# Performance work log

Measured on AMD Instinct MI355X. Metric: run time of the kernel, lower is better.

Reference implementation:

```python
import jax, jax.numpy as jnp
import numpy as np

NUM_HEADS = 12


def _rel_pos_table(q_size, k_size, rel_pos):
    # rel_pos: (2*q_size-1, head_dim); q_size == k_size here so no interpolation.
    q_coords = jnp.arange(q_size)[:, None] * max(k_size / q_size, 1.0)
    k_coords = jnp.arange(k_size)[None, :] * max(q_size / k_size, 1.0)
    rel = (q_coords - k_coords + (k_size - 1) * max(q_size / k_size, 1.0)).astype(jnp.int32)
    return rel_pos[rel]  # (q_size, k_size, head_dim)


def setup_inputs() -> dict:
    key = jax.random.key(0)
    ks = jax.random.split(key, 7)
    B, H, W, D = 1, 64, 64, 768
    hd = D // NUM_HEADS
    x = jax.random.normal(ks[0], (B, H, W, D), dtype=jnp.float32)
    w_qkv = jax.random.normal(ks[1], (3 * D, D), dtype=jnp.float32) * (1.0 / np.sqrt(D))
    b_qkv = jnp.zeros((3 * D,), dtype=jnp.float32)
    w_proj = jax.random.normal(ks[2], (D, D), dtype=jnp.float32) * (1.0 / np.sqrt(D))
    b_proj = jnp.zeros((D,), dtype=jnp.float32)
    rel_pos_h = jax.random.normal(ks[3], (2 * H - 1, hd), dtype=jnp.float32) * 0.02
    rel_pos_w = jax.random.normal(ks[4], (2 * W - 1, hd), dtype=jnp.float32) * 0.02
    return {"x": x, "w_qkv": w_qkv, "b_qkv": b_qkv, "w_proj": w_proj,
            "b_proj": b_proj, "rel_pos_h": rel_pos_h, "rel_pos_w": rel_pos_w}


def reference(x, w_qkv, b_qkv, w_proj, b_proj, rel_pos_h, rel_pos_w):
    b, h, w, d = x.shape
    nh = NUM_HEADS
    hd = d // nh
    scale = hd ** -0.5
    # combined qkv projection: (b,h,w,3d) -> (3, b*nh, h*w, hd)
    qkv = x @ w_qkv.T + b_qkv
    qkv = qkv.reshape(b, h * w, 3, nh, hd).transpose(2, 0, 3, 1, 4)
    qkv = qkv.reshape(3, b * nh, h * w, hd)
    q, k, v = qkv[0], qkv[1], qkv[2]
    attn = (q * scale) @ k.swapaxes(-2, -1)  # (b*nh, hw, hw)
    # decomposed 2D relative position bias
    rh = _rel_pos_table(h, h, rel_pos_h)  # (h, h, hd)
    rw = _rel_pos_table(w, w, rel_pos_w)  # (w, w, hd)
    r_q = q.reshape(b * nh, h, w, hd)
    rel_h = jnp.einsum('bhwc,hkc->bhwk', r_q, rh)
    rel_w = jnp.einsum('bhwc,wkc->bhwk', r_q, rw)
    attn = (attn.reshape(b * nh, h, w, h, w)
            + rel_h[:, :, :, :, None]
            + rel_w[:, :, :, None, :]).reshape(b * nh, h * w, h * w)
    attn = jax.nn.softmax(attn, axis=-1)
    out = attn @ v  # (b*nh, hw, hd)
    out = out.reshape(b, nh, h, w, hd).transpose(0, 2, 3, 1, 4).reshape(b, h, w, d)
    return out @ w_proj.T + b_proj
```

## Files before the change

### kernel.cpp

```cpp
#include <hip/hip_runtime.h>
#include <hip/hip_bf16.h>
#include <stdint.h>


typedef unsigned short u16;
typedef unsigned int   u32;
typedef __attribute__((ext_vector_type(8))) short s8v;
typedef __attribute__((ext_vector_type(4))) float f4v;
typedef __attribute__((ext_vector_type(4))) unsigned short us4;
typedef __attribute__((ext_vector_type(8))) unsigned short us8;
typedef __attribute__((ext_vector_type(2))) unsigned int u32x2;

#define DEVI static __device__ __forceinline__

constexpr int   NTOK   = 4096;
constexpr int   DM     = 768;
constexpr float LOG2E_F = 1.4426950408889634f;
constexpr float KSCALE  = 0.18033688011112042f;

#if __has_builtin(__builtin_amdgcn_exp2f)
#define EXP2(x) __builtin_amdgcn_exp2f(x)
#else
#define EXP2(x) exp2f(x)
#endif

DEVI u16 f2bf(float x){
  u32 u = __builtin_bit_cast(u32, x);
  u32 r = (u + 0x7FFFu + ((u >> 16) & 1u)) >> 16;
  return (u16)r;
}
DEVI float bf2f(u16 h){
  u32 u = ((u32)h) << 16;
  return __builtin_bit_cast(float, u);
}
DEVI u32 cvtpk(float lo, float hi){
  u32 r;
  asm("v_cvt_pk_bf16_f32 %0, %1, %2" : "=v"(r) : "v"(lo), "v"(hi));
  return r;
}

typedef const __attribute__((address_space(1))) u32* gp1;
typedef __attribute__((address_space(3))) u32* lp3;
DEVI void gload_lds16(const void* g, void* l){
  __builtin_amdgcn_global_load_lds((gp1)g, (lp3)l, 16, 0, 0);
}

DEVI f4v MFMA16(s8v a, s8v b, f4v c){
  return __builtin_amdgcn_mfma_f32_16x16x32_bf16(a, b, c, 0, 0, 0);
}

DEVI void hard_barrier(){
  __builtin_amdgcn_sched_barrier(0);
  asm volatile("" ::: "memory");
  __builtin_amdgcn_s_barrier();
  asm volatile("" ::: "memory");
  __builtin_amdgcn_sched_barrier(0);
}

__global__ void k_split(const float* __restrict__ in, u16* __restrict__ hi,
                        u16* __restrict__ lo, int n4){
  int i = blockIdx.x * blockDim.x + threadIdx.x;
  int stride = gridDim.x * blockDim.x;
  for (; i < n4; i += stride){
    f4v v = ((const f4v*)in)[i];
    us4 h, l;
#pragma unroll
    for (int j = 0; j < 4; ++j){
      u16 hb = f2bf(v[j]);
      h[j] = hb;
      l[j] = f2bf(v[j] - bf2f(hb));
    }
    ((us4*)hi)[i] = h;
    ((us4*)lo)[i] = l;
  }
}

template<int EPI>
__global__ __launch_bounds__(256)
void k_gemm(const u16* __restrict__ Ah, const u16* __restrict__ Al,
            const u16* __restrict__ Bh, const u16* __restrict__ Bl,
            const float* __restrict__ bias, int K,
            u16* __restrict__ Qh, u16* __restrict__ Ql,
            u16* __restrict__ Kh, u16* __restrict__ Kl,
            float* __restrict__ Vf, float* __restrict__ Cout)
{
  __shared__ __align__(16) unsigned char sm[65536];
  const int t = threadIdx.x;
  const int lane = t & 63, wid = t >> 6;
  const int l15 = lane & 15, g = lane >> 4;
  const int wr = wid >> 1, wc = wid & 1;
  const int m0 = blockIdx.y * 128, n0 = blockIdx.x * 128;

  const char* aGh[2]; const char* aGl[2]; const char* bGh[2]; const char* bGl[2];
#pragma unroll
  for (int ch = 0; ch < 2; ++ch){
    int p = ch * 4096 + t * 16;
    int pair = p >> 7, w = p & 127;
    int u = w ^ ((pair & 7) << 4);
    int row = 2 * pair + (u >> 6);
    int cb  = u & 63;
    aGh[ch] = (const char*)Ah + (size_t)(m0 + row) * K * 2 + cb;
    aGl[ch] = (const char*)Al + (size_t)(m0 + row) * K * 2 + cb;
    bGh[ch] = (const char*)Bh + (size_t)(n0 + row) * K * 2 + cb;
    bGl[ch] = (const char*)Bl + (size_t)(n0 + row) * K * 2 + cb;
  }
  const int axor = ((l15 & 1) * 64 + g * 16) ^ (((l15 >> 1) & 7) << 4);
  const int abase = (wr * 32 + (l15 >> 1)) * 128 + axor;
  const int bbase = 16384 + (wc * 32 + (l15 >> 1)) * 128 + axor;

#pragma unroll
  for (int ch = 0; ch < 2; ++ch){
    gload_lds16(aGh[ch], sm + 0     + ch*4096 + wid*1024);
    gload_lds16(aGl[ch], sm + 8192  + ch*4096 + wid*1024);
    gload_lds16(bGh[ch], sm + 16384 + ch*4096 + wid*1024);
    gload_lds16(bGl[ch], sm + 24576 + ch*4096 + wid*1024);
    aGh[ch] += 64; aGl[ch] += 64; bGh[ch] += 64; bGl[ch] += 64;
  }

  f4v acc[4][4] = {};
  const int KSTEPS = K >> 5;
  for (int kt = 0; kt < KSTEPS; ++kt){
    const int bb = (kt & 1) * 32768;
    if (kt + 1 < KSTEPS){
      const int nb = ((kt + 1) & 1) * 32768;
#pragma unroll
      for (int ch = 0; ch < 2; ++ch){
        gload_lds16(aGh[ch], sm + nb + 0     + ch*4096 + wid*1024);
        gload_lds16(aGl[ch], sm + nb + 8192  + ch*4096 + wid*1024);
        gload_lds16(bGh[ch], sm + nb + 16384 + ch*4096 + wid*1024);
        gload_lds16(bGl[ch], sm + nb + 24576 + ch*4096 + wid*1024);
        aGh[ch] += 64; aGl[ch] += 64; bGh[ch] += 64; bGl[ch] += 64;
      }
      asm volatile("s_waitcnt vmcnt(8)" ::: "memory");
    } else {
      asm volatile("s_waitcnt vmcnt(0)" ::: "memory");
    }
    hard_barrier();

    s8v af[4][2];
#pragma unroll
    for (int mi = 0; mi < 4; ++mi){
      af[mi][0] = *(const s8v*)(sm + bb + abase + mi*1024);
      af[mi][1] = *(const s8v*)(sm + bb + abase + mi*1024 + 8192);
    }
    __builtin_amdgcn_s_setprio(1);
#pragma unroll
    for (int ni = 0; ni < 4; ++ni){
      s8v bh = *(const s8v*)(sm + bb + bbase + ni*1024);
      s8v bl = *(const s8v*)(sm + bb + bbase + ni*1024 + 8192);
#pragma unroll
      for (int mi = 0; mi < 4; ++mi){
        acc[mi][ni] = MFMA16(af[mi][0], bh, acc[mi][ni]);
        acc[mi][ni] = MFMA16(af[mi][0], bl, acc[mi][ni]);
        acc[mi][ni] = MFMA16(af[mi][1], bh, acc[mi][ni]);
      }
    }
    __builtin_amdgcn_s_setprio(0);
    hard_barrier();
  }

  if (EPI == 2){
#pragma unroll
    for (int ni = 0; ni < 4; ++ni){
      int col = n0 + wc*64 + ni*16 + l15;
      float bq = bias[col];
#pragma unroll
      for (int mi = 0; mi < 4; ++mi){
        int rw0 = m0 + wr*64 + mi*16 + g*4;
#pragma unroll
        for (int r = 0; r < 4; ++r)
          Cout[(size_t)(rw0 + r) * DM + col] = acc[mi][ni][r] + bq;
      }
    }
  } else {
#pragma unroll
    for (int ni = 0; ni < 4; ++ni){
      int colb = n0 + wc*64 + ni*16;
      float bq = bias[colb + l15];
      int which = colb / DM;
      int rem   = colb % DM;
      int head  = rem >> 6;
      int c     = (rem & 63) + l15;
#pragma unroll
      for (int mi = 0; mi < 4; ++mi){
        int n = m0 + wr*64 + mi*16 + g*4;
#pragma unroll
        for (int r = 0; r < 4; ++r){
          float v = acc[mi][ni][r] + bq;
          size_t idx = ((size_t)head * NTOK + (n + r)) * 64 + c;
          if (which == 0){
            u16 hb = f2bf(v);
            Qh[idx] = hb; Ql[idx] = f2bf(v - bf2f(hb));
          } else if (which == 1){
            float v2 = v * KSCALE;
            u16 hb = f2bf(v2);
            Kh[idx] = hb; Kl[idx] = f2bf(v2 - bf2f(hb));
          } else {
            Vf[idx] = v;
          }
        }
      }
    }
  }
}

__global__ void k_vtrans(const float* __restrict__ Vf, u16* __restrict__ Vth){
  __shared__ float tile[64][65];
  int h = blockIdx.y, nt = blockIdx.x;
  int t = threadIdx.x;
  {
    int r = t >> 2, c0 = (t & 3) * 16;
    const float* src = Vf + ((size_t)h * NTOK + nt*64 + r) * 64 + c0;
#pragma unroll
    for (int j = 0; j < 4; ++j){
      f4v v = *(const f4v*)(src + j*4);
      tile[r][c0+j*4+0] = v[0]; tile[r][c0+j*4+1] = v[1];
      tile[r][c0+j*4+2] = v[2]; tile[r][c0+j*4+3] = v[3];
    }
  }
  __syncthreads();
  {
    int c = t >> 2, b = (t & 3) * 16;
    us8 o0, o1;
#pragma unroll
    for (int i = 0; i < 16; ++i){
      u16 bv = f2bf(tile[b + i][c]);
      if (i < 8) o0[i] = bv; else o1[i-8] = bv;
    }
    u16* dst = Vth + ((size_t)h * 64 + c) * NTOK + nt*64 + b;
    *(us8*)(dst)     = o0;
    *(us8*)(dst + 8) = o1;
  }
}

__global__ void k_relh(const u16* __restrict__ Qh, const u16* __restrict__ Ql,
                       const float* __restrict__ rp, float* __restrict__ R){
  __shared__ float qs[64][68];
  __shared__ float rs[64][68];
  int h = blockIdx.y, qh = blockIdx.x;
  int t = threadIdx.x;
  {
    int r = t >> 2, c0 = (t & 3) * 16;
    size_t qb = ((size_t)h * NTOK + qh*64 + r) * 64 + c0;
#pragma unroll
    for (int j = 0; j < 2; ++j){
      us8 vh = *(const us8*)(Qh + qb + j*8);
      us8 vl = *(const us8*)(Ql + qb + j*8);
#pragma unroll
      for (int e = 0; e < 8; ++e)
        qs[r][c0 + j*8 + e] = bf2f(vh[e]) + bf2f(vl[e]);
    }
    const float* pr = rp + (size_t)(qh - r + 63) * 64 + c0;
#pragma unroll
    for (int j = 0; j < 4; ++j){
      f4v v = *(const f4v*)(pr + j*4);
      rs[r][c0+j*4+0]=v[0]; rs[r][c0+j*4+1]=v[1];
      rs[r][c0+j*4+2]=v[2]; rs[r][c0+j*4+3]=v[3];
    }
  }
  __syncthreads();
  int qw = t >> 2, k0 = t & 3;
  float acc[16] = {};
  for (int c = 0; c < 64; c += 4){
    f4v qv = *(const f4v*)(&qs[qw][c]);
#pragma unroll
    for (int i = 0; i < 16; ++i){
      f4v rv = *(const f4v*)(&rs[k0 + 4*i][c]);
      acc[i] += qv[0]*rv[0] + qv[1]*rv[1] + qv[2]*rv[2] + qv[3]*rv[3];
    }
  }
  float* o = R + ((size_t)h * NTOK + qh*64 + qw) * 64;
#pragma unroll
  for (int i = 0; i < 16; ++i) o[k0 + 4*i] = acc[i] * LOG2E_F;
}

__global__ void k_relw(const u16* __restrict__ Qh, const u16* __restrict__ Ql,
                       const float* __restrict__ rp, float* __restrict__ R){
  __shared__ float qs[64][68];
  __shared__ float rs[64][68];
  int h = blockIdx.y, qw = blockIdx.x;
  int t = threadIdx.x;
  {
    int r = t >> 2, c0 = (t & 3) * 16;
    size_t qb = ((size_t)h * NTOK + r*64 + qw) * 64 + c0;
#pragma unroll
    for (int j = 0; j < 2; ++j){
      us8 vh = *(const us8*)(Qh + qb + j*8);
      us8 vl = *(const us8*)(Ql + qb + j*8);
#pragma unroll
      for (int e = 0; e < 8; ++e)
        qs[r][c0 + j*8 + e] = bf2f(vh[e]) + bf2f(vl[e]);
    }
    const float* pr = rp + (size_t)(qw - r + 63) * 64 + c0;
#pragma unroll
    for (int j = 0; j < 4; ++j){
      f4v v = *(const f4v*)(pr + j*4);
      rs[r][c0+j*4+0]=v[0]; rs[r][c0+j*4+1]=v[1];
      rs[r][c0+j*4+2]=v[2]; rs[r][c0+j*4+3]=v[3];
    }
  }
  __syncthreads();
  int qh = t >> 2, k0 = t & 3;
  float acc[16] = {};
  for (int c = 0; c < 64; c += 4){
    f4v qv = *(const f4v*)(&qs[qh][c]);
#pragma unroll
    for (int i = 0; i < 16; ++i){
      f4v rv = *(const f4v*)(&rs[k0 + 4*i][c]);
      acc[i] += qv[0]*rv[0] + qv[1]*rv[1] + qv[2]*rv[2] + qv[3]*rv[3];
    }
  }
  float* o = R + ((size_t)h * NTOK + qh*64 + qw) * 64;
#pragma unroll
  for (int i = 0; i < 16; ++i) o[k0 + 4*i] = acc[i] * LOG2E_F;
}

__global__ __launch_bounds__(256)
void k_attn(const u16* __restrict__ Qh, const u16* __restrict__ Ql,
            const u16* __restrict__ Kh, const u16* __restrict__ Kl,
            const u16* __restrict__ Vth,
            const float* __restrict__ Rh, const float* __restrict__ Rw,
            u16* __restrict__ Oh, u16* __restrict__ Ol)
{
  constexpr int BUF1 = 24576, POFF = 49152, RHOFF = 58368;
  __shared__ __align__(16) unsigned char sm[75776];
  const int t = threadIdx.x;
  const int lane = t & 63, wid = t >> 6;
  const int l15 = lane & 15, g = lane >> 4;
  const int h = blockIdx.y;
  const int qrow0 = blockIdx.x * 64 + wid * 16;

  const char* kGh[2]; const char* kGl[2]; const char* vG[2];
#pragma unroll
  for (int ch = 0; ch < 2; ++ch){
    int p = ch * 4096 + t * 16;
    int row = p >> 7;
    int cb  = (p & 127) ^ ((row & 7) << 4);
    kGh[ch] = (const char*)Kh + ((size_t)h * NTOK + row) * 128 + cb;
    kGl[ch] = (const char*)Kl + ((size_t)h * NTOK + row) * 128 + cb;
    vG[ch]  = (const char*)Vth + ((size_t)h * 64 + row) * (NTOK*2) + cb;
  }

  {
    const char* rhg = (const char*)(Rh + ((size_t)h * NTOK + blockIdx.x * 64) * 64);
#pragma unroll
    for (int s2 = 0; s2 < 4; ++s2){
      int off = s2*4096 + t*16;
      f4v v = *(const f4v*)(rhg + off);
      *(f4v*)(sm + RHOFF + (off >> 8) * 272 + (off & 255)) = v;
    }
  }
  asm volatile("s_waitcnt lgkmcnt(0)" ::: "memory");

  const size_t qoff = ((size_t)h * NTOK + qrow0 + l15) * 64 + g * 8;
  s8v qh0 = *(const s8v*)(Qh + qoff);
  s8v qh1 = *(const s8v*)(Qh + qoff + 32);
  s8v ql0 = *(const s8v*)(Ql + qoff);
  s8v ql1 = *(const s8v*)(Ql + qoff + 32);

  const int xr  = (l15 & 7) << 4;
  const int kb0 = l15 * 128 + ((g * 16)      ^ xr);
  const int kb1 = l15 * 128 + ((g * 16 + 64) ^ xr);
  const int vb0 = 16384 + kb0;
  const int vb1 = 16384 + kb1;
  const int pbase = POFF + wid * 2304 + l15 * 144;
  const int rhrd  = RHOFF + (wid * 16 + l15) * 272;

  const float* rwp = Rw + ((size_t)h * NTOK + qrow0 + l15) * 64 + 4*g;
  f4v rwv[4];
#pragma unroll
  for (int tt = 0; tt < 4; ++tt) rwv[tt] = *(const f4v*)(rwp + 16*tt);

#pragma unroll
  for (int ch = 0; ch < 2; ++ch){
    gload_lds16(kGh[ch], sm + 0     + ch*4096 + wid*1024);
    gload_lds16(kGl[ch], sm + 8192  + ch*4096 + wid*1024);
    gload_lds16(vG[ch],  sm + 16384 + ch*4096 + wid*1024);
    kGh[ch] += 8192; kGl[ch] += 8192; vG[ch] += 128;
  }

  f4v o[4] = {};
  float m2 = -1.0e30f, ls = 0.f;

  for (int it = 0; it < 64; ++it){
    const int bb = (it & 1) * BUF1;
    if (it < 63){
      const int nb = ((it + 1) & 1) * BUF1;
#pragma unroll
      for (int ch = 0; ch < 2; ++ch){
        gload_lds16(kGh[ch], sm + nb + 0     + ch*4096 + wid*1024);
        gload_lds16(kGl[ch], sm + nb + 8192  + ch*4096 + wid*1024);
        gload_lds16(vG[ch],  sm + nb + 16384 + ch*4096 + wid*1024);
        kGh[ch] += 8192; kGl[ch] += 8192; vG[ch] += 128;
      }
      asm volatile("s_waitcnt vmcnt(6)" ::: "memory");
    } else {
      asm volatile("s_waitcnt vmcnt(0)" ::: "memory");
    }
    hard_barrier();

    const float rhv = *(const float*)(sm + rhrd + it * 4);

    f4v s[4];
    __builtin_amdgcn_s_setprio(1);
#pragma unroll
    for (int tt = 0; tt < 4; ++tt){
      s8v kh_0 = *(const s8v*)(sm + bb + kb0 + tt*2048);
      s8v kh_1 = *(const s8v*)(sm + bb + kb1 + tt*2048);
      s8v kl_0 = *(const s8v*)(sm + bb + kb0 + tt*2048 + 8192);
      s8v kl_1 = *(const s8v*)(sm + bb + kb1 + tt*2048 + 8192);
      f4v a = {};
      a = MFMA16(kh_0, qh0, a);
      a = MFMA16(kh_1, qh1, a);
      a = MFMA16(kl_0, qh0, a);
      a = MFMA16(kl_1, qh1, a);
      a = MFMA16(kh_0, ql0, a);
      a = MFMA16(kh_1, ql1, a);
      s[tt] = a;
    }
    __builtin_amdgcn_s_setprio(0);

    float pm = -1.0e30f;
#pragma unroll
    for (int tt = 0; tt < 4; ++tt){
#pragma unroll
      for (int r = 0; r < 4; ++r){
        s[tt][r] += rhv + rwv[tt][r];
        pm = fmaxf(pm, s[tt][r]);
      }
    }
    pm = fmaxf(pm, __shfl_xor(pm, 16, 64));
    pm = fmaxf(pm, __shfl_xor(pm, 32, 64));
    const float mn = fmaxf(m2, pm);
    const float fr = EXP2(m2 - mn);
    m2 = mn;
    float ps = 0.f;
#pragma unroll
    for (int tt = 0; tt < 4; ++tt){
#pragma unroll
      for (int r = 0; r < 4; ++r){
        float p = EXP2(s[tt][r] - m2);
        s[tt][r] = p;
        ps += p;
      }
    }
    ps += __shfl_xor(ps, 16, 64);
    ps += __shfl_xor(ps, 32, 64);
    ls = ls * fr + ps;

#pragma unroll
    for (int tt = 0; tt < 4; ++tt){
      u32x2 w2;
      w2[0] = cvtpk(s[tt][0], s[tt][1]);
      w2[1] = cvtpk(s[tt][2], s[tt][3]);
      *(u32x2*)(sm + pbase + 8*g + 32*tt) = w2;
    }
#pragma unroll
    for (int dt = 0; dt < 4; ++dt){
#pragma unroll
      for (int r = 0; r < 4; ++r) o[dt][r] *= fr;
    }
    s8v pa0 = *(const s8v*)(sm + pbase + 16*g);
    s8v pa1 = *(const s8v*)(sm + pbase + 16*g + 64);
    __builtin_amdgcn_s_setprio(1);
#pragma unroll
    for (int dt = 0; dt < 4; ++dt){
      s8v v0 = *(const s8v*)(sm + bb + vb0 + dt*2048);
      s8v v1 = *(const s8v*)(sm + bb + vb1 + dt*2048);
      o[dt] = MFMA16(v0, pa0, o[dt]);
      o[dt] = MFMA16(v1, pa1, o[dt]);
    }
    __builtin_amdgcn_s_setprio(0);

    hard_barrier();
  }

  const float inv = 1.0f / ls;
  const size_t obase = (size_t)(qrow0 + l15) * DM + h*64 + 4*g;
#pragma unroll
  for (int dt = 0; dt < 4; ++dt){
    us4 hv, lv;
#pragma unroll
    for (int r = 0; r < 4; ++r){
      float v = o[dt][r] * inv;
      u16 hb = f2bf(v);
      hv[r] = hb;
      lv[r] = f2bf(v - bf2f(hb));
    }
    *(us4*)(Oh + obase + 16*dt) = hv;
    *(us4*)(Ol + obase + 16*dt) = lv;
  }
}

extern "C" void kernel_launch(void* const* d_in, const int* in_sizes, int n_in,
                              void* d_out, int out_size, void* d_ws, size_t ws_size,
                              hipStream_t stream){
  (void)in_sizes; (void)n_in; (void)out_size; (void)ws_size;
  const float* x      = (const float*)d_in[0];
  const float* w_qkv  = (const float*)d_in[1];
  const float* b_qkv  = (const float*)d_in[2];
  const float* w_proj = (const float*)d_in[3];
  const float* b_proj = (const float*)d_in[4];
  const float* rph    = (const float*)d_in[5];
  const float* rpw    = (const float*)d_in[6];
  float* out = (float*)d_out;

  char* w = (char*)d_ws;
  size_t off = 0;
  auto nxt = [&](size_t b) -> char* {
    char* p = w + off; off += (b + 255) & ~(size_t)255; return p;
  };
  u16*   Xh  = (u16*)  nxt((size_t)NTOK*DM*2);
  u16*   Xl  = (u16*)  nxt((size_t)NTOK*DM*2);
  u16*   Wqh = (u16*)  nxt((size_t)3*DM*DM*2);
  u16*   Wql = (u16*)  nxt((size_t)3*DM*DM*2);
  u16*   Wph = (u16*)  nxt((size_t)DM*DM*2);
  u16*   Wpl = (u16*)  nxt((size_t)DM*DM*2);
  u16*   Qh  = (u16*)  nxt((size_t)NTOK*DM*2);
  u16*   Ql  = (u16*)  nxt((size_t)NTOK*DM*2);
  u16*   Kh  = (u16*)  nxt((size_t)NTOK*DM*2);
  u16*   Kl  = (u16*)  nxt((size_t)NTOK*DM*2);
  float* Vf  = (float*)nxt((size_t)NTOK*DM*4);
  u16*   Vth = (u16*)  nxt((size_t)NTOK*DM*2);
  float* Rh  = (float*)nxt((size_t)12*NTOK*64*4);
  float* Rw  = (float*)nxt((size_t)12*NTOK*64*4);
  u16*   Oh  = Xh;
  u16*   Ol  = Xl;

  k_split<<<dim3(3072), dim3(256), 0, stream>>>(x,      Xh,  Xl,  NTOK*DM/4);
  k_split<<<dim3(1728), dim3(256), 0, stream>>>(w_qkv,  Wqh, Wql, 3*DM*DM/4);
  k_split<<<dim3(576),  dim3(256), 0, stream>>>(w_proj, Wph, Wpl, DM*DM/4);

  k_gemm<1><<<dim3(18, 32), dim3(256), 0, stream>>>(
      Xh, Xl, Wqh, Wql, b_qkv, DM, Qh, Ql, Kh, Kl, Vf, nullptr);

  k_vtrans<<<dim3(64, 12), dim3(256), 0, stream>>>(Vf, Vth);
  k_relh  <<<dim3(64, 12), dim3(256), 0, stream>>>(Qh, Ql, rph, Rh);
  k_relw  <<<dim3(64, 12), dim3(256), 0, stream>>>(Qh, Ql, rpw, Rw);

  k_attn<<<dim3(64, 12), dim3(256), 0, stream>>>(Qh, Ql, Kh, Kl, Vth, Rh, Rw, Oh, Ol);

  k_gemm<2><<<dim3(6, 32), dim3(256), 0, stream>>>(
      Oh, Ol, Wph, Wpl, b_proj, DM,
      nullptr, nullptr, nullptr, nullptr, nullptr, out);
}
```

Before: 373.5 us.

## Replace LDS double-buffer direct loads with single-buffer register-staged prefetch

The attention kernel drops its double-buffered global-to-LDS direct loads and uses a single LDS buffer. The next K/V tile is prefetched into registers during compute and written to LDS after a barrier. The Rh bias is now read from global memory each iteration instead of being staged in LDS. Shared memory falls from about 74 KB to 33 KB, which could allow more blocks per CU, at the cost of extra VGPRs, a second barrier per iteration and a scalar global load in the loop.

```diff
diff --git a/kernel.cpp b/kernel.cpp
--- a/kernel.cpp
+++ b/kernel.cpp
@@ -322,8 +322,7 @@
             const float* __restrict__ Rh, const float* __restrict__ Rw,
             u16* __restrict__ Oh, u16* __restrict__ Ol)
 {
-  constexpr int BUF1 = 24576, POFF = 49152, RHOFF = 58368;
-  __shared__ __align__(16) unsigned char sm[75776];
+  __shared__ __align__(16) unsigned char sm[33792];
   const int t = threadIdx.x;
   const int lane = t & 63, wid = t >> 6;
   const int l15 = lane & 15, g = lane >> 4;
@@ -341,17 +340,6 @@
     vG[ch]  = (const char*)Vth + ((size_t)h * 64 + row) * (NTOK*2) + cb;
   }
 
-  {
-    const char* rhg = (const char*)(Rh + ((size_t)h * NTOK + blockIdx.x * 64) * 64);
-#pragma unroll
-    for (int s2 = 0; s2 < 4; ++s2){
-      int off = s2*4096 + t*16;
-      f4v v = *(const f4v*)(rhg + off);
-      *(f4v*)(sm + RHOFF + (off >> 8) * 272 + (off & 255)) = v;
-    }
-  }
-  asm volatile("s_waitcnt lgkmcnt(0)" ::: "memory");
-
   const size_t qoff = ((size_t)h * NTOK + qrow0 + l15) * 64 + g * 8;
   s8v qh0 = *(const s8v*)(Qh + qoff);
   s8v qh1 = *(const s8v*)(Qh + qoff + 32);
@@ -363,52 +351,52 @@
   const int kb1 = l15 * 128 + ((g * 16 + 64) ^ xr);
   const int vb0 = 16384 + kb0;
   const int vb1 = 16384 + kb1;
-  const int pbase = POFF + wid * 2304 + l15 * 144;
-  const int rhrd  = RHOFF + (wid * 16 + l15) * 272;
+  const int pbase = 24576 + wid * 2304 + l15 * 144;
 
   const float* rwp = Rw + ((size_t)h * NTOK + qrow0 + l15) * 64 + 4*g;
   f4v rwv[4];
 #pragma unroll
   for (int tt = 0; tt < 4; ++tt) rwv[tt] = *(const f4v*)(rwp + 16*tt);
-
-#pragma unroll
-  for (int ch = 0; ch < 2; ++ch){
-    gload_lds16(kGh[ch], sm + 0     + ch*4096 + wid*1024);
-    gload_lds16(kGl[ch], sm + 8192  + ch*4096 + wid*1024);
-    gload_lds16(vG[ch],  sm + 16384 + ch*4096 + wid*1024);
-    kGh[ch] += 8192; kGl[ch] += 8192; vG[ch] += 128;
-  }
+  const float* rhp = Rh + ((size_t)h * NTOK + qrow0 + l15) * 64;
+
+  f4v st[6];
+  auto do_loads = [&](){
+    st[0] = *(const f4v*)kGh[0]; st[1] = *(const f4v*)kGh[1];
+    st[2] = *(const f4v*)kGl[0]; st[3] = *(const f4v*)kGl[1];
+    st[4] = *(const f4v*)vG[0];  st[5] = *(const f4v*)vG[1];
+    kGh[0] += 8192; kGh[1] += 8192;
+    kGl[0] += 8192; kGl[1] += 8192;
+    vG[0]  += 128;  vG[1]  += 128;
+  };
+  auto do_writes = [&](){
+    *(f4v*)(sm + 0     +    0 + t*16) = st[0];
+    *(f4v*)(sm + 0     + 4096 + t*16) = st[1];
+    *(f4v*)(sm + 8192  +    0 + t*16) = st[2];
+    *(f4v*)(sm + 8192  + 4096 + t*16) = st[3];
+    *(f4v*)(sm + 16384 +    0 + t*16) = st[4];
+    *(f4v*)(sm + 16384 + 4096 + t*16) = st[5];
+  };
+
+  do_loads();
+  do_writes();
+  do_loads();
+  asm volatile("s_waitcnt lgkmcnt(0)" ::: "memory");
+  hard_barrier();
 
   f4v o[4] = {};
   float m2 = -1.0e30f, ls = 0.f;
 
   for (int it = 0; it < 64; ++it){
-    const int bb = (it & 1) * BUF1;
-    if (it < 63){
-      const int nb = ((it + 1) & 1) * BUF1;
-#pragma unroll
-      for (int ch = 0; ch < 2; ++ch){
-        gload_lds16(kGh[ch], sm + nb + 0     + ch*4096 + wid*1024);
-        gload_lds16(kGl[ch], sm + nb + 8192  + ch*4096 + wid*1024);
-        gload_lds16(vG[ch],  sm + nb + 16384 + ch*4096 + wid*1024);
-        kGh[ch] += 8192; kGl[ch] += 8192; vG[ch] += 128;
-      }
-      asm volatile("s_waitcnt vmcnt(6)" ::: "memory");
-    } else {
-      asm volatile("s_waitcnt vmcnt(0)" ::: "memory");
-    }
-    hard_barrier();
-
-    const float rhv = *(const float*)(sm + rhrd + it * 4);
+    const float rhv = rhp[it];
 
     f4v s[4];
     __builtin_amdgcn_s_setprio(1);
 #pragma unroll
     for (int tt = 0; tt < 4; ++tt){
-      s8v kh_0 = *(const s8v*)(sm + bb + kb0 + tt*2048);
-      s8v kh_1 = *(const s8v*)(sm + bb + kb1 + tt*2048);
-      s8v kl_0 = *(const s8v*)(sm + bb + kb0 + tt*2048 + 8192);
-      s8v kl_1 = *(const s8v*)(sm + bb + kb1 + tt*2048 + 8192);
+      s8v kh_0 = *(const s8v*)(sm + kb0 + tt*2048);
+      s8v kh_1 = *(const s8v*)(sm + kb1 + tt*2048);
+      s8v kl_0 = *(const s8v*)(sm + kb0 + tt*2048 + 8192);
+      s8v kl_1 = *(const s8v*)(sm + kb1 + tt*2048 + 8192);
       f4v a = {};
       a = MFMA16(kh_0, qh0, a);
       a = MFMA16(kh_1, qh1, a);
@@ -465,13 +453,19 @@
     __builtin_amdgcn_s_setprio(1);
 #pragma unroll
     for (int dt = 0; dt < 4; ++dt){
-      s8v v0 = *(const s8v*)(sm + bb + vb0 + dt*2048);
-      s8v v1 = *(const s8v*)(sm + bb + vb1 + dt*2048);
+      s8v v0 = *(const s8v*)(sm + vb0 + dt*2048);
+      s8v v1 = *(const s8v*)(sm + vb1 + dt*2048);
       o[dt] = MFMA16(v0, pa0, o[dt]);
       o[dt] = MFMA16(v1, pa1, o[dt]);
     }
     __builtin_amdgcn_s_setprio(0);
 
+    hard_barrier();
+    if (it < 63){
+      do_writes();
+      if (it < 62) do_loads();
+    }
+    asm volatile("s_waitcnt lgkmcnt(0)" ::: "memory");
     hard_barrier();
   }
 
```

Result: faster. 348.1 us (-6.8%).
